# Kernel optimization log

Hardware: AMD Instinct MI355X
Metric: run time of the kernel (lower is better)

Reference implementation:

```python
import jax, jax.numpy as jnp
import numpy as np

N_NODES = 100000
N_EDGES = 1600000
IN_DIM = 64
HIDDEN = 128
CLASSES = 3
N_MATERIALS = 8


def setup_inputs() -> dict:
    key = jax.random.key(0)
    ks = jax.random.split(key, 12)
    def lin(k, fan_in, fan_out):
        bound = 1.0 / np.sqrt(fan_in)
        kw, kb = jax.random.split(k)
        W = jax.random.uniform(kw, (fan_in, fan_out), jnp.float32, -bound, bound)
        b = jax.random.uniform(kb, (fan_out,), jnp.float32, -bound, bound)
        return W, b
    x = jax.random.normal(ks[0], (N_NODES, IN_DIM), jnp.float32)
    edge_index = jax.random.randint(ks[1], (2, N_EDGES), 0, N_NODES, jnp.int64)
    Wl1, b1 = lin(ks[2], IN_DIM, HIDDEN)   # SAGEConv lin_l (agg, with bias)
    Wr1, _ = lin(ks[3], IN_DIM, HIDDEN)    # SAGEConv lin_r (root, no bias)
    Wl2, b2 = lin(ks[4], HIDDEN, HIDDEN)
    Wr2, _ = lin(ks[5], HIDDEN, HIDDEN)
    Wh, bh = lin(ks[6], HIDDEN, CLASSES)
    Wm, bm = lin(ks[7], HIDDEN, N_MATERIALS)
    return {"x": x, "edge_index": edge_index,
            "Wl1": Wl1, "Wr1": Wr1, "b1": b1,
            "Wl2": Wl2, "Wr2": Wr2, "b2": b2,
            "Wh": Wh, "bh": bh, "Wm": Wm, "bm": bm}


def _sage_conv(x, src, dst, Wl, Wr, b, n_nodes):
    # mean-aggregate source features at destination nodes, then linear + root linear
    msg = x[src]                                               # [E, F]
    agg = jax.ops.segment_sum(msg, dst, num_segments=n_nodes)  # [N, F]
    deg = jax.ops.segment_sum(jnp.ones((src.shape[0],), x.dtype), dst,
                              num_segments=n_nodes)            # [N]
    agg = agg / jnp.maximum(deg, 1.0)[:, None]
    return agg @ Wl + x @ Wr + b


def reference(x, edge_index, Wl1, Wr1, b1, Wl2, Wr2, b2, Wh, bh, Wm, bm):
    src, dst = edge_index[0], edge_index[1]
    n = x.shape[0]
    h = jax.nn.relu(_sage_conv(x, src, dst, Wl1, Wr1, b1, n))
    # dropout(p=0.35) is identity in eval mode
    h = jax.nn.relu(_sage_conv(h, src, dst, Wl2, Wr2, b2, n))
    return (h @ Wh + bh, h @ Wm + bm)
```

## Files before the change

### kernel.cpp

```cpp
#include <hip/hip_runtime.h>

#define N_NODES 100000
#define N_EDGES 1600000
#define NBUCK 391
#define BSH 8
#define EPT 32

typedef __attribute__((ext_vector_type(8))) short short8;
typedef __attribute__((ext_vector_type(4))) float f32x4;

__device__ __forceinline__ float bflo(unsigned int u) { return __uint_as_float(u << 16); }
__device__ __forceinline__ float bfhi(unsigned int u) { return __uint_as_float(u & 0xffff0000u); }
__device__ __forceinline__ float bf2f(unsigned short u) { return __uint_as_float(((unsigned int)u) << 16); }
__device__ __forceinline__ unsigned short f2bf(float f) {
    unsigned int u = __float_as_uint(f);
    return (unsigned short)((u + 0x7fffu + ((u >> 16) & 1u)) >> 16);
}

__global__ __launch_bounds__(256) void k_cast_hist_pack(
    const float* __restrict__ x, unsigned short* __restrict__ xh,
    const int* __restrict__ dst, int* __restrict__ deg,
    const float* __restrict__ Wl1, const float* __restrict__ Wr1,
    const float* __restrict__ Wl2, const float* __restrict__ Wr2,
    unsigned short* __restrict__ Bp1, unsigned short* __restrict__ Bp2)
{
    if (blockIdx.x < 6250) {
        int i = blockIdx.x * 256 + threadIdx.x;
        float4 v = *reinterpret_cast<const float4*>(x + (size_t)i * 4);
        ushort4 o;
        o.x = f2bf(v.x); o.y = f2bf(v.y); o.z = f2bf(v.z); o.w = f2bf(v.w);
        *reinterpret_cast<ushort4*>(xh + (size_t)i * 4) = o;
        atomicAdd(&deg[dst[i]], 1);
    } else {
        int idx = (blockIdx.x - 6250) * 256 + threadIdx.x;
        if (idx < 16384) {
            int j = idx & 7, g = (idx >> 3) & 3, col = (idx >> 5) & 127, kk = idx >> 12;
            int r = kk * 32 + g * 8 + j;
            float w = (r < 64) ? Wl1[r * 128 + col] : Wr1[(r - 64) * 128 + col];
            Bp1[idx] = f2bf(w);
        } else {
            int q = idx - 16384;
            int j = q & 7, g = (q >> 3) & 3, col = (q >> 5) & 127, kk = q >> 12;
            int r = kk * 32 + g * 8 + j;
            float w = (r < 128) ? Wl2[r * 128 + col] : Wr2[(r - 128) * 128 + col];
            Bp2[q] = f2bf(w);
        }
    }
}

__global__ __launch_bounds__(1024) void k_part_scan(const int* __restrict__ deg,
                                                    int* __restrict__ rowstart, int* __restrict__ bsum) {
    __shared__ int wsum[16];
    const int tid = threadIdx.x, lane = tid & 63, wid = tid >> 6;
    int i = blockIdx.x * 1024 + tid;
    int v = (i < N_NODES) ? deg[i] : 0;
    int s = v;
    #pragma unroll
    for (int off = 1; off < 64; off <<= 1) {
        int t = __shfl_up(s, off);
        if (lane >= off) s += t;
    }
    if (lane == 63) wsum[wid] = s;
    __syncthreads();
    if (tid < 16) {
        int w = wsum[tid];
        #pragma unroll
        for (int off = 1; off < 16; off <<= 1) {
            int t = __shfl_up(w, off);
            if (tid >= off) w += t;
        }
        wsum[tid] = w;
    }
    __syncthreads();
    int wexcl = (wid == 0) ? 0 : wsum[wid - 1];
    if (i < N_NODES) rowstart[i] = wexcl + s - v;
    if (tid == 1023) bsum[blockIdx.x] = wexcl + s;
}

__global__ __launch_bounds__(128) void k_scan_bsum(const int* __restrict__ bsum, int* __restrict__ boff,
                                                   int* __restrict__ rowstart, int* __restrict__ ccur, int nblk) {
    __shared__ int sh[128];
    __shared__ int excl[128];
    int t = threadIdx.x;
    int v = (t < nblk) ? bsum[t] : 0;
    int acc = v;
    sh[t] = acc;
    __syncthreads();
    #pragma unroll
    for (int off = 1; off < 128; off <<= 1) {
        int add = (t >= off) ? sh[t - off] : 0;
        __syncthreads();
        acc += add;
        sh[t] = acc;
        __syncthreads();
    }
    if (t < nblk) boff[t] = acc - v;
    excl[t] = acc - v;
    if (t == nblk - 1) rowstart[N_NODES] = acc;
    __syncthreads();
    for (int c = t; c < NBUCK; c += 128)
        ccur[c] = rowstart[c << BSH] + excl[c >> 2];
}

__global__ __launch_bounds__(1024) void k_add_off(const int* __restrict__ boff, int* __restrict__ rowstart) {
    int i = blockIdx.x * 1024 + threadIdx.x;
    if (i < N_NODES) rowstart[i] += boff[blockIdx.x];
}

__global__ __launch_bounds__(256) void k_bucket(const int* __restrict__ src, const int* __restrict__ dst,
                                                int* __restrict__ ccur, unsigned int* __restrict__ pairs) {
    __shared__ int cnt[NBUCK];
    __shared__ int base[NBUCK];
    const int tid = threadIdx.x;
    const int e_base = blockIdx.x * (256 * EPT);
    for (int i = tid; i < NBUCK; i += 256) cnt[i] = 0;
    __syncthreads();
    #pragma unroll
    for (int i = 0; i < EPT; ++i) {
        int e = e_base + i * 256 + tid;
        if (e < N_EDGES) atomicAdd(&cnt[dst[e] >> BSH], 1);
    }
    __syncthreads();
    for (int i = tid; i < NBUCK; i += 256) {
        int c = cnt[i];
        base[i] = (c > 0) ? atomicAdd(&ccur[i], c) : 0;
        cnt[i] = 0;
    }
    __syncthreads();
    #pragma unroll
    for (int i = 0; i < EPT; ++i) {
        int e = e_base + i * 256 + tid;
        if (e < N_EDGES) {
            int d = dst[e];
            int bkt = d >> BSH;
            int off = atomicAdd(&cnt[bkt], 1);
            pairs[base[bkt] + off] = ((unsigned int)(d & 255) << 17) | (unsigned int)src[e];
        }
    }
}

__global__ __launch_bounds__(256) void k_scatter_csr(const int* __restrict__ rowstart,
                                                     const unsigned int* __restrict__ pairs,
                                                     int* __restrict__ srcs) {
    __shared__ int lcur[256];
    const int c = blockIdx.x, tid = threadIdx.x;
    const int nbase = c << BSH;
    {
        int n = nbase + tid;
        lcur[tid] = (n < N_NODES) ? rowstart[n] : 0;
    }
    __syncthreads();
    int e0 = rowstart[nbase];
    int nend = nbase + 256; if (nend > N_NODES) nend = N_NODES;
    int e1 = rowstart[nend];
    for (int e = e0 + tid; e < e1; e += 256) {
        unsigned int u = pairs[e];
        int dloc = (int)(u >> 17);
        int p = atomicAdd(&lcur[dloc], 1);
        srcs[p] = (int)(u & 0x1FFFFu);
    }
}

__global__ __launch_bounds__(256, 8) void k_layer1(
    const unsigned short* __restrict__ xh,
    const int* __restrict__ rowstart, const int* __restrict__ srcs,
    const unsigned short* __restrict__ Bp1, const float* __restrict__ b,
    unsigned short* __restrict__ h1h)
{
    __shared__ unsigned short A[32][136];
    __shared__ int rs[33];
    const int tile = blockIdx.x * 32;
    const int tid = threadIdx.x, lane = tid & 63, wid = tid >> 6;

    if (tid < 33) rs[tid] = rowstart[tile + tid];
    {
        int node = tid >> 3, part = tid & 7;
        uint4 v = *reinterpret_cast<const uint4*>(xh + (size_t)(tile + node) * 64 + part * 8);
        *reinterpret_cast<uint4*>(&A[node][64 + part * 8]) = v;
    }
    __syncthreads();

    for (int it = 0; it < 8; ++it) {
        int nl = wid * 8 + it;
        int e0 = rs[nl], e1 = rs[nl + 1];
        float a0 = 0.f, a1 = 0.f, a2 = 0.f, a3 = 0.f;
        int e = e0;
        for (; e + 8 <= e1; e += 8) {
            int s0 = srcs[e],     s1 = srcs[e + 1], s2 = srcs[e + 2], s3 = srcs[e + 3];
            int s4 = srcs[e + 4], s5 = srcs[e + 5], s6 = srcs[e + 6], s7 = srcs[e + 7];
            float v0 = bf2f(xh[(size_t)s0 * 64 + lane]);
            float v1 = bf2f(xh[(size_t)s1 * 64 + lane]);
            float v2 = bf2f(xh[(size_t)s2 * 64 + lane]);
            float v3 = bf2f(xh[(size_t)s3 * 64 + lane]);
            float v4 = bf2f(xh[(size_t)s4 * 64 + lane]);
            float v5 = bf2f(xh[(size_t)s5 * 64 + lane]);
            float v6 = bf2f(xh[(size_t)s6 * 64 + lane]);
            float v7 = bf2f(xh[(size_t)s7 * 64 + lane]);
            a0 += v0; a1 += v1; a2 += v2; a3 += v3;
            a0 += v4; a1 += v5; a2 += v6; a3 += v7;
        }
        for (; e < e1; ++e)
            a0 += bf2f(xh[(size_t)srcs[e] * 64 + lane]);
        float acc = (a0 + a1) + (a2 + a3);
        int d = e1 - e0;
        A[nl][lane] = f2bf(acc * ((d > 0) ? (1.0f / (float)d) : 1.0f));
    }
    __syncthreads();

    const int r15 = lane & 15, g4 = lane >> 4;
    const int n0 = wid * 32;
    f32x4 acc[2][2] = {};
    for (int kk = 0; kk < 4; ++kk) {
        short8 b0 = *reinterpret_cast<const short8*>(Bp1 + (((kk * 128 + n0 + r15) * 4 + g4) << 3));
        short8 b1 = *reinterpret_cast<const short8*>(Bp1 + (((kk * 128 + n0 + 16 + r15) * 4 + g4) << 3));
        #pragma unroll
        for (int mt = 0; mt < 2; ++mt) {
            short8 a = *reinterpret_cast<const short8*>(&A[mt * 16 + r15][kk * 32 + g4 * 8]);
            acc[mt][0] = __builtin_amdgcn_mfma_f32_16x16x32_bf16(a, b0, acc[mt][0], 0, 0, 0);
            acc[mt][1] = __builtin_amdgcn_mfma_f32_16x16x32_bf16(a, b1, acc[mt][1], 0, 0, 0);
        }
    }
    #pragma unroll
    for (int mt = 0; mt < 2; ++mt)
        #pragma unroll
        for (int nt = 0; nt < 2; ++nt) {
            int col = n0 + nt * 16 + r15;
            float bb = b[col];
            #pragma unroll
            for (int reg = 0; reg < 4; ++reg) {
                int row = tile + mt * 16 + g4 * 4 + reg;
                h1h[(size_t)row * 128 + col] = f2bf(fmaxf(acc[mt][nt][reg] + bb, 0.0f));
            }
        }
}

__global__ __launch_bounds__(256, 8) void k_layer2(
    const unsigned int* __restrict__ h1h32,
    const int* __restrict__ rowstart, const int* __restrict__ srcs,
    const unsigned short* __restrict__ Bp2, const float* __restrict__ b,
    const float* __restrict__ Wh, const float* __restrict__ bh,
    const float* __restrict__ Wm, const float* __restrict__ bm,
    float* __restrict__ out1, float* __restrict__ out2)
{
    __shared__ unsigned short A[32][264];
    __shared__ int rs[33];
    const int tile = blockIdx.x * 32;
    const int tid = threadIdx.x, lane = tid & 63, wid = tid >> 6;

    if (tid < 33) rs[tid] = rowstart[tile + tid];
    {
        int node = tid >> 3, part = tid & 7;
        const unsigned int* p = h1h32 + (size_t)(tile + node) * 64 + part * 8;
        uint4 v0 = *reinterpret_cast<const uint4*>(p);
        uint4 v1 = *reinterpret_cast<const uint4*>(p + 4);
        *reinterpret_cast<uint4*>(&A[node][128 + part * 16]) = v0;
        *reinterpret_cast<uint4*>(&A[node][128 + part * 16 + 8]) = v1;
    }
    __syncthreads();

    for (int it = 0; it < 8; ++it) {
        int nl = wid * 8 + it;
        int e0 = rs[nl], e1 = rs[nl + 1];
        float ax0 = 0.f, ax1 = 0.f, ax2 = 0.f, ax3 = 0.f;
        float ay0 = 0.f, ay1 = 0.f, ay2 = 0.f, ay3 = 0.f;
        int e = e0;
        for (; e + 8 <= e1; e += 8) {
            int s0 = srcs[e],     s1 = srcs[e + 1], s2 = srcs[e + 2], s3 = srcs[e + 3];
            int s4 = srcs[e + 4], s5 = srcs[e + 5], s6 = srcs[e + 6], s7 = srcs[e + 7];
            unsigned int u0 = h1h32[(size_t)s0 * 64 + lane];
            unsigned int u1 = h1h32[(size_t)s1 * 64 + lane];
            unsigned int u2 = h1h32[(size_t)s2 * 64 + lane];
            unsigned int u3 = h1h32[(size_t)s3 * 64 + lane];
            unsigned int u4 = h1h32[(size_t)s4 * 64 + lane];
            unsigned int u5 = h1h32[(size_t)s5 * 64 + lane];
            unsigned int u6 = h1h32[(size_t)s6 * 64 + lane];
            unsigned int u7 = h1h32[(size_t)s7 * 64 + lane];
            ax0 += bflo(u0); ay0 += bfhi(u0);
            ax1 += bflo(u1); ay1 += bfhi(u1);
            ax2 += bflo(u2); ay2 += bfhi(u2);
            ax3 += bflo(u3); ay3 += bfhi(u3);
            ax0 += bflo(u4); ay0 += bfhi(u4);
            ax1 += bflo(u5); ay1 += bfhi(u5);
            ax2 += bflo(u6); ay2 += bfhi(u6);
            ax3 += bflo(u7); ay3 += bfhi(u7);
        }
        for (; e < e1; ++e) {
            unsigned int u = h1h32[(size_t)srcs[e] * 64 + lane];
            ax0 += bflo(u); ay0 += bfhi(u);
        }
        float ax = (ax0 + ax1) + (ax2 + ax3);
        float ay = (ay0 + ay1) + (ay2 + ay3);
        int d = e1 - e0;
        float rd = (d > 0) ? (1.0f / (float)d) : 1.0f;
        unsigned int p = (unsigned int)f2bf(ax * rd) | ((unsigned int)f2bf(ay * rd) << 16);
        *reinterpret_cast<unsigned int*>(&A[nl][2 * lane]) = p;
    }
    __syncthreads();

    const int r15 = lane & 15, g4 = lane >> 4;
    const int n0 = wid * 32;
    f32x4 acc[2][2] = {};
    for (int kk = 0; kk < 8; ++kk) {
        short8 b0 = *reinterpret_cast<const short8*>(Bp2 + (((kk * 128 + n0 + r15) * 4 + g4) << 3));
        short8 b1 = *reinterpret_cast<const short8*>(Bp2 + (((kk * 128 + n0 + 16 + r15) * 4 + g4) << 3));
        #pragma unroll
        for (int mt = 0; mt < 2; ++mt) {
            short8 a = *reinterpret_cast<const short8*>(&A[mt * 16 + r15][kk * 32 + g4 * 8]);
            acc[mt][0] = __builtin_amdgcn_mfma_f32_16x16x32_bf16(a, b0, acc[mt][0], 0, 0, 0);
            acc[mt][1] = __builtin_amdgcn_mfma_f32_16x16x32_bf16(a, b1, acc[mt][1], 0, 0, 0);
        }
    }
    __syncthreads();
    float* h2L = reinterpret_cast<float*>(&A[0][0]);
    #pragma unroll
    for (int mt = 0; mt < 2; ++mt)
        #pragma unroll
        for (int nt = 0; nt < 2; ++nt) {
            int col = n0 + nt * 16 + r15;
            float bb = b[col];
            #pragma unroll
            for (int reg = 0; reg < 4; ++reg) {
                int row = mt * 16 + g4 * 4 + reg;
                h2L[row * 132 + col] = fmaxf(acc[mt][nt][reg] + bb, 0.0f);
            }
        }
    __syncthreads();

    for (int t = tid; t < 352; t += 256) {
        int node = t / 11, o = t - node * 11;
        const float* h2 = &h2L[node * 132];
        if (o < 3) {
            float s = bh[o];
            for (int k = 0; k < 128; ++k) s += h2[k] * Wh[k * 3 + o];
            out1[(size_t)(tile + node) * 3 + o] = s;
        } else {
            int m = o - 3;
            float s = bm[m];
            for (int k = 0; k < 128; ++k) s += h2[k] * Wm[k * 8 + m];
            out2[(size_t)(tile + node) * 8 + m] = s;
        }
    }
}

extern "C" void kernel_launch(void* const* d_in, const int* in_sizes, int n_in,
                              void* d_out, int out_size, void* d_ws, size_t ws_size,
                              hipStream_t stream) {
    const float* x   = (const float*)d_in[0];
    const int*   ei  = (const int*)d_in[1];
    const int*   src = ei;
    const int*   dst = ei + N_EDGES;
    const float* Wl1 = (const float*)d_in[2];
    const float* Wr1 = (const float*)d_in[3];
    const float* b1  = (const float*)d_in[4];
    const float* Wl2 = (const float*)d_in[5];
    const float* Wr2 = (const float*)d_in[6];
    const float* b2  = (const float*)d_in[7];
    const float* Wh  = (const float*)d_in[8];
    const float* bh  = (const float*)d_in[9];
    const float* Wm  = (const float*)d_in[10];
    const float* bm  = (const float*)d_in[11];

    float* out1 = (float*)d_out;
    float* out2 = out1 + (size_t)N_NODES * 3;

    char* ws = (char*)d_ws;
    int*   deg      = (int*)(ws);
    int*   rowstart = (int*)(ws + (512 << 10));
    int*   bsum     = (int*)(ws + (960 << 10));
    int*   boff     = (int*)(ws + (1024 << 10));
    int*   ccur     = (int*)(ws + (1088 << 10));
    unsigned int* pairs = (unsigned int*)(ws + (1536 << 10));
    int*   srcs     = (int*)(ws + (8192 << 10));
    unsigned short* xh  = (unsigned short*)(ws + (15360 << 10));
    unsigned short* h1h = (unsigned short*)(ws + (28672 << 10));
    unsigned short* Bp1 = (unsigned short*)(ws + (54784 << 10));
    unsigned short* Bp2 = (unsigned short*)(ws + (54848 << 10));

    const int NSCAN = (N_NODES + 1023) / 1024;
    const int NBKT_BLKS = (N_EDGES + 256 * EPT - 1) / (256 * EPT);

    hipMemsetAsync(deg, 0, N_NODES * sizeof(int), stream);
    k_cast_hist_pack<<<6442, 256, 0, stream>>>(x, xh, dst, deg, Wl1, Wr1, Wl2, Wr2, Bp1, Bp2);
    k_part_scan<<<NSCAN, 1024, 0, stream>>>(deg, rowstart, bsum);
    k_scan_bsum<<<1, 128, 0, stream>>>(bsum, boff, rowstart, ccur, NSCAN);
    k_add_off<<<NSCAN, 1024, 0, stream>>>(boff, rowstart);
    k_bucket<<<NBKT_BLKS, 256, 0, stream>>>(src, dst, ccur, pairs);
    k_scatter_csr<<<NBUCK, 256, 0, stream>>>(rowstart, pairs, srcs);

    k_layer1<<<3125, 256, 0, stream>>>(xh, rowstart, srcs, Bp1, b1, h1h);
    k_layer2<<<3125, 256, 0, stream>>>((const unsigned int*)h1h, rowstart, srcs,
                                       Bp2, b2, Wh, bh, Wm, bm, out1, out2);
}
```

Before: 317.5 us.

## Build CSR from bucket histogram and compute per-node offsets inside bucket kernel

Replaces the per-node global degree histogram and three-kernel multi-block scan with a coarse per-bucket histogram, computed with shared-memory atomics, followed by a single-block 391-entry scan. Per-node row starts are now derived inside the CSR scatter kernel through a local histogram and block scan over each bucket's pairs. This removes 1.6M global atomics, two kernel launches and a large memset. In exchange the CSR kernel reads the pairs twice. EPT is also doubled, which halves the number of bucket blocks.

```diff
diff --git a/kernel.cpp b/kernel.cpp
--- a/kernel.cpp
+++ b/kernel.cpp
@@ -4,7 +4,7 @@
 #define N_EDGES 1600000
 #define NBUCK 391
 #define BSH 8
-#define EPT 32
+#define EPT 64
 
 typedef __attribute__((ext_vector_type(8))) short short8;
 typedef __attribute__((ext_vector_type(4))) float f32x4;
@@ -17,22 +17,38 @@
     return (unsigned short)((u + 0x7fffu + ((u >> 16) & 1u)) >> 16);
 }
 
-__global__ __launch_bounds__(256) void k_cast_hist_pack(
+__global__ __launch_bounds__(256) void k_pre(
     const float* __restrict__ x, unsigned short* __restrict__ xh,
-    const int* __restrict__ dst, int* __restrict__ deg,
+    const int* __restrict__ dst, int* __restrict__ bcnt,
     const float* __restrict__ Wl1, const float* __restrict__ Wr1,
     const float* __restrict__ Wl2, const float* __restrict__ Wr2,
     unsigned short* __restrict__ Bp1, unsigned short* __restrict__ Bp2)
 {
+    __shared__ int hcnt[NBUCK];
+    const int tid = threadIdx.x;
     if (blockIdx.x < 6250) {
-        int i = blockIdx.x * 256 + threadIdx.x;
+        int i = blockIdx.x * 256 + tid;
         float4 v = *reinterpret_cast<const float4*>(x + (size_t)i * 4);
         ushort4 o;
         o.x = f2bf(v.x); o.y = f2bf(v.y); o.z = f2bf(v.z); o.w = f2bf(v.w);
         *reinterpret_cast<ushort4*>(xh + (size_t)i * 4) = o;
-        atomicAdd(&deg[dst[i]], 1);
+    } else if (blockIdx.x < 6348) {
+        int blk = blockIdx.x - 6250;
+        int e_base = blk * (256 * EPT);
+        for (int i = tid; i < NBUCK; i += 256) hcnt[i] = 0;
+        __syncthreads();
+        #pragma unroll
+        for (int i = 0; i < EPT; ++i) {
+            int e = e_base + i * 256 + tid;
+            if (e < N_EDGES) atomicAdd(&hcnt[dst[e] >> BSH], 1);
+        }
+        __syncthreads();
+        for (int i = tid; i < NBUCK; i += 256) {
+            int c = hcnt[i];
+            if (c > 0) atomicAdd(&bcnt[i], c);
+        }
     } else {
-        int idx = (blockIdx.x - 6250) * 256 + threadIdx.x;
+        int idx = (blockIdx.x - 6348) * 256 + tid;
         if (idx < 16384) {
             int j = idx & 7, g = (idx >> 3) & 3, col = (idx >> 5) & 127, kk = idx >> 12;
             int r = kk * 32 + g * 8 + j;
@@ -48,12 +64,11 @@
     }
 }
 
-__global__ __launch_bounds__(1024) void k_part_scan(const int* __restrict__ deg,
-                                                    int* __restrict__ rowstart, int* __restrict__ bsum) {
-    __shared__ int wsum[16];
+__global__ __launch_bounds__(512) void k_scan391(const int* __restrict__ bcnt,
+                                                 int* __restrict__ bbase, int* __restrict__ ccur) {
+    __shared__ int wsum[8];
     const int tid = threadIdx.x, lane = tid & 63, wid = tid >> 6;
-    int i = blockIdx.x * 1024 + tid;
-    int v = (i < N_NODES) ? deg[i] : 0;
+    int v = (tid < NBUCK) ? bcnt[tid] : 0;
     int s = v;
     #pragma unroll
     for (int off = 1; off < 64; off <<= 1) {
@@ -62,49 +77,19 @@
     }
     if (lane == 63) wsum[wid] = s;
     __syncthreads();
-    if (tid < 16) {
+    if (tid < 8) {
         int w = wsum[tid];
         #pragma unroll
-        for (int off = 1; off < 16; off <<= 1) {
+        for (int off = 1; off < 8; off <<= 1) {
             int t = __shfl_up(w, off);
             if (tid >= off) w += t;
         }
         wsum[tid] = w;
     }
     __syncthreads();
-    int wexcl = (wid == 0) ? 0 : wsum[wid - 1];
-    if (i < N_NODES) rowstart[i] = wexcl + s - v;
-    if (tid == 1023) bsum[blockIdx.x] = wexcl + s;
-}
-
-__global__ __launch_bounds__(128) void k_scan_bsum(const int* __restrict__ bsum, int* __restrict__ boff,
-                                                   int* __restrict__ rowstart, int* __restrict__ ccur, int nblk) {
-    __shared__ int sh[128];
-    __shared__ int excl[128];
-    int t = threadIdx.x;
-    int v = (t < nblk) ? bsum[t] : 0;
-    int acc = v;
-    sh[t] = acc;
-    __syncthreads();
-    #pragma unroll
-    for (int off = 1; off < 128; off <<= 1) {
-        int add = (t >= off) ? sh[t - off] : 0;
-        __syncthreads();
-        acc += add;
-        sh[t] = acc;
-        __syncthreads();
-    }
-    if (t < nblk) boff[t] = acc - v;
-    excl[t] = acc - v;
-    if (t == nblk - 1) rowstart[N_NODES] = acc;
-    __syncthreads();
-    for (int c = t; c < NBUCK; c += 128)
-        ccur[c] = rowstart[c << BSH] + excl[c >> 2];
-}
-
-__global__ __launch_bounds__(1024) void k_add_off(const int* __restrict__ boff, int* __restrict__ rowstart) {
-    int i = blockIdx.x * 1024 + threadIdx.x;
-    if (i < N_NODES) rowstart[i] += boff[blockIdx.x];
+    int excl = ((wid == 0) ? 0 : wsum[wid - 1]) + s - v;
+    if (tid < NBUCK + 1) bbase[tid] = excl;
+    if (tid < NBUCK) ccur[tid] = excl;
 }
 
 __global__ __launch_bounds__(256) void k_bucket(const int* __restrict__ src, const int* __restrict__ dst,
@@ -139,24 +124,49 @@
     }
 }
 
-__global__ __launch_bounds__(256) void k_scatter_csr(const int* __restrict__ rowstart,
-                                                     const unsigned int* __restrict__ pairs,
-                                                     int* __restrict__ srcs) {
-    __shared__ int lcur[256];
-    const int c = blockIdx.x, tid = threadIdx.x;
+__global__ __launch_bounds__(256) void k_csr(const int* __restrict__ bbase,
+                                             const unsigned int* __restrict__ pairs,
+                                             int* __restrict__ rowstart, int* __restrict__ srcs) {
+    __shared__ int nh[256];
+    __shared__ int wsum[4];
+    const int c = blockIdx.x, tid = threadIdx.x, lane = tid & 63, wid = tid >> 6;
     const int nbase = c << BSH;
-    {
-        int n = nbase + tid;
-        lcur[tid] = (n < N_NODES) ? rowstart[n] : 0;
-    }
-    __syncthreads();
-    int e0 = rowstart[nbase];
-    int nend = nbase + 256; if (nend > N_NODES) nend = N_NODES;
-    int e1 = rowstart[nend];
+    const int e0 = bbase[c], e1 = bbase[c + 1];
+
+    nh[tid] = 0;
+    __syncthreads();
+    for (int e = e0 + tid; e < e1; e += 256)
+        atomicAdd(&nh[pairs[e] >> 17], 1);
+    __syncthreads();
+    int v = nh[tid];
+    int s = v;
+    #pragma unroll
+    for (int off = 1; off < 64; off <<= 1) {
+        int t = __shfl_up(s, off);
+        if (lane >= off) s += t;
+    }
+    if (lane == 63) wsum[wid] = s;
+    __syncthreads();
+    if (tid < 4) {
+        int w = wsum[tid];
+        #pragma unroll
+        for (int off = 1; off < 4; off <<= 1) {
+            int t = __shfl_up(w, off);
+            if (tid >= off) w += t;
+        }
+        wsum[tid] = w;
+    }
+    __syncthreads();
+    int excl = e0 + ((wid == 0) ? 0 : wsum[wid - 1]) + s - v;
+    int n = nbase + tid;
+    if (n < N_NODES) rowstart[n] = excl;
+    if (c == NBUCK - 1 && tid == 0) rowstart[N_NODES] = bbase[NBUCK];
+    __syncthreads();
+    nh[tid] = excl;
+    __syncthreads();
     for (int e = e0 + tid; e < e1; e += 256) {
         unsigned int u = pairs[e];
-        int dloc = (int)(u >> 17);
-        int p = atomicAdd(&lcur[dloc], 1);
+        int p = atomicAdd(&nh[u >> 17], 1);
         srcs[p] = (int)(u & 0x1FFFFu);
     }
 }
@@ -364,11 +374,10 @@
     float* out2 = out1 + (size_t)N_NODES * 3;
 
     char* ws = (char*)d_ws;
-    int*   deg      = (int*)(ws);
+    int*   bcnt     = (int*)(ws);
+    int*   bbase    = (int*)(ws + (64 << 10));
+    int*   ccur     = (int*)(ws + (128 << 10));
     int*   rowstart = (int*)(ws + (512 << 10));
-    int*   bsum     = (int*)(ws + (960 << 10));
-    int*   boff     = (int*)(ws + (1024 << 10));
-    int*   ccur     = (int*)(ws + (1088 << 10));
     unsigned int* pairs = (unsigned int*)(ws + (1536 << 10));
     int*   srcs     = (int*)(ws + (8192 << 10));
     unsigned short* xh  = (unsigned short*)(ws + (15360 << 10));
@@ -376,16 +385,13 @@
     unsigned short* Bp1 = (unsigned short*)(ws + (54784 << 10));
     unsigned short* Bp2 = (unsigned short*)(ws + (54848 << 10));
 
-    const int NSCAN = (N_NODES + 1023) / 1024;
     const int NBKT_BLKS = (N_EDGES + 256 * EPT - 1) / (256 * EPT);
 
-    hipMemsetAsync(deg, 0, N_NODES * sizeof(int), stream);
-    k_cast_hist_pack<<<6442, 256, 0, stream>>>(x, xh, dst, deg, Wl1, Wr1, Wl2, Wr2, Bp1, Bp2);
-    k_part_scan<<<NSCAN, 1024, 0, stream>>>(deg, rowstart, bsum);
-    k_scan_bsum<<<1, 128, 0, stream>>>(bsum, boff, rowstart, ccur, NSCAN);
-    k_add_off<<<NSCAN, 1024, 0, stream>>>(boff, rowstart);
+    hipMemsetAsync(bcnt, 0, NBUCK * sizeof(int), stream);
+    k_pre<<<6540, 256, 0, stream>>>(x, xh, dst, bcnt, Wl1, Wr1, Wl2, Wr2, Bp1, Bp2);
+    k_scan391<<<1, 512, 0, stream>>>(bcnt, bbase, ccur);
     k_bucket<<<NBKT_BLKS, 256, 0, stream>>>(src, dst, ccur, pairs);
-    k_scatter_csr<<<NBUCK, 256, 0, stream>>>(rowstart, pairs, srcs);
+    k_csr<<<NBUCK, 256, 0, stream>>>(bbase, pairs, rowstart, srcs);
 
     k_layer1<<<3125, 256, 0, stream>>>(xh, rowstart, srcs, Bp1, b1, h1h);
     k_layer2<<<3125, 256, 0, stream>>>((const unsigned int*)h1h, rowstart, srcs,
```

Result: faster. 301.6 us (-5.0%).
